# Optimization experiments

Hardware: AMD Instinct MI355X
Metric: run time of the kernel (lower is better)

The kernel has to match this reference:

```python
import jax, jax.numpy as jnp
import numpy as np

WS, SS, IMG, NH = 7, 3, 56, 6  # window, shift, image size, heads
N = WS * WS                    # tokens per window = 49


def _rel_pos_index():
    coords = np.stack(np.meshgrid(np.arange(WS), np.arange(WS), indexing='ij')).reshape(2, -1)
    rel = (coords[:, :, None] - coords[:, None, :]).transpose(1, 2, 0)  # (N,N,2)
    rel[..., 0] += WS - 1
    rel[..., 1] += WS - 1
    rel[..., 0] *= 2 * WS - 1
    return rel.sum(-1)  # (N,N) int


def _attn_mask():
    m = np.zeros((IMG, IMG), np.float32)
    sl = (slice(0, -WS), slice(-WS, -SS), slice(-SS, None))
    cnt = 0
    for hs in sl:
        for ws_ in sl:
            m[hs, ws_] = cnt
            cnt += 1
    mw = m.reshape(IMG // WS, WS, IMG // WS, WS).transpose(0, 2, 1, 3).reshape(-1, N)  # (nW,N)
    diff = mw[:, None, :] - mw[:, :, None]
    return np.where(diff != 0, -100.0, 0.0).astype(np.float32)  # (nW,N,N)


def _ln(x, g, b, eps=1e-5):
    mu = x.mean(-1, keepdims=True)
    var = ((x - mu) ** 2).mean(-1, keepdims=True)
    return (x - mu) * jax.lax.rsqrt(var + eps) * g + b


def reference(x, rpb_table, w_qkv, b_qkv, w_proj, b_proj, g0, be0, g1, be1, w_fc1, b_fc1, w_fc2, b_fc2):
    B, C, _, _ = x.shape
    dh = C // NH
    nWs = IMG // WS
    nW = nWs * nWs

    xs = x.transpose(0, 2, 3, 1)            # NHWC [B,IMG,IMG,C]
    shortcut = xs
    h = _ln(xs, g0, be0)
    h = jnp.roll(h, (-SS, -SS), axis=(1, 2))
    # window partition -> [B*nW, N, C]
    h = h.reshape(B, nWs, WS, nWs, WS, C).transpose(0, 1, 3, 2, 4, 5).reshape(B * nW, N, C)

    qkv = h @ w_qkv.T + b_qkv               # [B_,N,3C]
    qkv = qkv.reshape(B * nW, N, dh, NH, 3)  # matches torch reshape (b_,N,C//h,h,3)
    q = qkv[..., 0].transpose(0, 3, 1, 2) * (dh ** -0.5)  # [B_,H,N,dh]
    k = qkv[..., 1].transpose(0, 3, 1, 2)
    v = qkv[..., 2].transpose(0, 3, 1, 2)

    att = jnp.einsum('bhnd,bhmd->bhnm', q, k)             # [B_,H,N,N]
    bias = rpb_table[jnp.asarray(_rel_pos_index().reshape(-1))].reshape(N, N, NH).transpose(2, 0, 1)
    att = att + bias[None]
    mask = jnp.asarray(_attn_mask())                      # [nW,N,N]
    att = att.reshape(B, nW, NH, N, N) + mask[None, :, None]
    att = jax.nn.softmax(att.reshape(B * nW, NH, N, N), axis=-1)

    o = jnp.einsum('bhnm,bhmd->bnhd', att, v).reshape(B * nW, WS, WS, C)
    o = o @ w_proj.T + b_proj
    # window reverse -> [B,IMG,IMG,C]
    o = o.reshape(B, nWs, nWs, WS, WS, C).transpose(0, 1, 3, 2, 4, 5).reshape(B, IMG, IMG, C)
    o = jnp.roll(o, (SS, SS), axis=(1, 2))

    xs = shortcut + o
    h2 = _ln(xs, g1, be1)
    h2 = jax.nn.gelu(h2 @ w_fc1.T + b_fc1, approximate=False) @ w_fc2.T + b_fc2
    xs = xs + h2
    return xs.transpose(0, 3, 1, 2)  # back to NCHW


def setup_inputs() -> dict:
    key = jax.random.key(0)
    ks = jax.random.split(key, 8)
    C, Hn = 192, 768
    return {
        'x': jax.random.normal(ks[0], (64, C, 56, 56), jnp.float32),
        'rpb_table': jax.random.normal(ks[1], (169, NH), jnp.float32) * 0.02,
        'w_qkv': jax.random.normal(ks[2], (3 * C, C), jnp.float32) * 0.02,
        'b_qkv': jnp.zeros((3 * C,), jnp.float32),
        'w_proj': jax.random.normal(ks[3], (C, C), jnp.float32) * 0.02,
        'b_proj': jnp.zeros((C,), jnp.float32),
        'g0': jnp.ones((C,), jnp.float32),
        'be0': jnp.zeros((C,), jnp.float32),
        'g1': jnp.ones((C,), jnp.float32),
        'be1': jnp.zeros((C,), jnp.float32),
        'w_fc1': jax.random.normal(ks[4], (Hn, C), jnp.float32) * 0.02,
        'b_fc1': jnp.zeros((Hn,), jnp.float32),
        'w_fc2': jax.random.normal(ks[5], (C, Hn), jnp.float32) * 0.02,
        'b_fc2': jnp.zeros((C,), jnp.float32),
    }
```

## Files before the change

kernel.cpp:

```cpp
#include <hip/hip_runtime.h>
#include <hip/hip_bf16.h>

typedef unsigned short ushortT;
typedef __attribute__((ext_vector_type(8))) short short8;
typedef __attribute__((ext_vector_type(4))) float f32x4;
typedef __attribute__((address_space(3))) unsigned int lds_uint;
typedef __attribute__((address_space(1))) const unsigned int glob_uint;

#define MFMA16(a,b,c) __builtin_amdgcn_mfma_f32_16x16x32_bf16(a,b,c,0,0,0)

__device__ __forceinline__ ushortT f2bf(float f){
  union {float f; unsigned u;} v; v.f = f;
  unsigned r = v.u + 0x7FFFu + ((v.u >> 16) & 1u);
  return (ushortT)(r >> 16);
}
__device__ __forceinline__ float bf2f(ushortT u){
  union {unsigned u; float f;} v; v.u = ((unsigned)u) << 16; return v.f;
}
__device__ __forceinline__ float gelu_f(float v){
  float u = 0.7978845608028654f * (v + 0.044715f*v*v*v);
  float e = __expf(2.0f*u);
  return 0.5f * v * (1.0f + (1.0f - 2.0f/(e + 1.0f)));
}

#define SCALE_Q 0.17677669529663687f

__global__ void k_prep(const float* __restrict__ rpb, const float* __restrict__ wqkv,
                       const float* __restrict__ bqkv, const float* __restrict__ wproj,
                       const float* __restrict__ wfc1, const float* __restrict__ wfc2,
                       ushortT* __restrict__ wqkvp, float* __restrict__ bqkvp,
                       ushortT* __restrict__ wprojb, ushortT* __restrict__ wfc1b,
                       ushortT* __restrict__ wfc2b, float* __restrict__ bm)
{
  int i = blockIdx.x * 256 + threadIdx.x;
  if (i < 110592){
    int rp = i / 192, c = i % 192;
    int s = rp / 192, rem = rp % 192, hh = rem / 32, d = rem % 32;
    int rin = d*18 + hh*3 + s;
    float v = wqkv[rin*192 + c];
    if (s == 0) v *= SCALE_Q;
    wqkvp[i] = f2bf(v);
    return;
  }
  i -= 110592;
  if (i < 576){
    int rp = i;
    int s = rp / 192, rem = rp % 192, hh = rem / 32, d = rem % 32;
    int rin = d*18 + hh*3 + s;
    float v = bqkv[rin];
    if (s == 0) v *= SCALE_Q;
    bqkvp[i] = v;
    return;
  }
  i -= 576;
  if (i < 36864){ wprojb[i] = f2bf(wproj[i]); return; }
  i -= 36864;
  if (i < 147456){ wfc1b[i] = f2bf(wfc1[i]); return; }
  i -= 147456;
  if (i < 147456){ wfc2b[i] = f2bf(wfc2[i]); return; }
  i -= 147456;
  if (i < 921984){
    int j = i % 49; int t = i / 49; int ii = t % 49; t /= 49; int hh = t % 6; int w = t / 6;
    int r1 = ii/7, c1 = ii%7, r2 = j/7, c2 = j%7;
    int idx = (r1 - r2 + 6)*13 + (c1 - c2 + 6);
    float bias = rpb[idx*6 + hh];
    int wy = w >> 3, wx = w & 7;
    int hi = wy*7 + r1, wi = wx*7 + c1, hj = wy*7 + r2, wj = wx*7 + c2;
    int regi = 3*((hi<49)?0:((hi<53)?1:2)) + ((wi<49)?0:((wi<53)?1:2));
    int regj = 3*((hj<49)?0:((hj<53)?1:2)) + ((wj<49)?0:((wj<53)?1:2));
    bm[i] = bias + ((regi != regj) ? -100.0f : 0.0f);
  }
}

__global__ void k_tr(const float* __restrict__ x, ushortT* __restrict__ xsb)
{
  __shared__ float tile[192*57];
  int bh = blockIdx.x; int b = bh / 56, h = bh % 56;
  const float* src = x + (size_t)b*602112 + (size_t)h*56;
  for (int e = threadIdx.x; e < 192*56; e += 256){
    int c = e / 56, w = e % 56;
    tile[c*57 + w] = src[(size_t)c*3136 + w];
  }
  __syncthreads();
  ushortT* dst = xsb + (size_t)bh*56*192;
  for (int e = threadIdx.x; e < 56*192; e += 256){
    int w = e / 192, c = e % 192;
    dst[(size_t)w*192 + c] = f2bf(tile[c*57 + w]);
  }
}

__global__ __launch_bounds__(256,2) void k_attn(
  ushortT* __restrict__ xsb, const ushortT* __restrict__ wqkvp, const float* __restrict__ bqkvp,
  const ushortT* __restrict__ wprojb, const float* __restrict__ bproj,
  const float* __restrict__ g0, const float* __restrict__ be0,
  const float* __restrict__ g1, const float* __restrict__ be1,
  const float* __restrict__ bm, ushortT* __restrict__ xs2b)
{
  __shared__ ushortT ln0[49][200];
  __shared__ ushortT ks[49][200];
  __shared__ ushortT vT[6][32][72];
  __shared__ ushortT Pw[4][16][72];

  const int tid = threadIdx.x;
  const int lane = tid & 63, wv = tid >> 6;
  const int l15 = lane & 15, g = lane >> 4;
  const int wid = blockIdx.x;
  const int b = wid >> 6, wloc = wid & 63, wy = wloc >> 3, wx = wloc & 7;
  const int mbase = wv * 16;

  unsigned xr01[13]; ushortT xr2[13];
  #pragma unroll
  for (int it = 0; it < 13; it++){
    int t = wv + it*4;
    if (t < 49){
      int r = t / 7, cc = t % 7;
      int hsrc = (wy*7 + r + 3) % 56;
      int wsrc = (wx*7 + cc + 3) % 56;
      const ushortT* px = xsb + ((size_t)((b*56 + hsrc)*56 + wsrc))*192;
      ushortT r0 = px[lane], r1 = px[lane+64], r2 = px[lane+128];
      xr01[it] = ((unsigned)r1 << 16) | r0; xr2[it] = r2;
      float x0 = bf2f(r0), x1 = bf2f(r1), x2 = bf2f(r2);
      float s = x0 + x1 + x2, sq = x0*x0 + x1*x1 + x2*x2;
      #pragma unroll
      for (int m = 1; m < 64; m <<= 1){ s += __shfl_xor(s, m, 64); sq += __shfl_xor(sq, m, 64); }
      float mu = s * (1.0f/192.0f);
      float var = sq * (1.0f/192.0f) - mu*mu;
      float rs = rsqrtf(var + 1e-5f);
      ln0[t][lane]     = f2bf((x0-mu)*rs*g0[lane]     + be0[lane]);
      ln0[t][lane+64]  = f2bf((x1-mu)*rs*g0[lane+64]  + be0[lane+64]);
      ln0[t][lane+128] = f2bf((x2-mu)*rs*g0[lane+128] + be0[lane+128]);
    }
  }
  __syncthreads();

  {
    short8 a[4][6];
    #pragma unroll
    for (int mt = 0; mt < 4; mt++){
      int ra = mt*16 + l15; if (ra > 48) ra = 48;
      #pragma unroll
      for (int kc = 0; kc < 6; kc++)
        a[mt][kc] = *(const short8*)(&ln0[ra][kc*32 + g*8]);
    }
    __syncthreads();
    for (int ntl = 0; ntl < 9; ntl++){
      int nt = wv*9 + ntl;
      int cp = nt*16 + l15;
      const ushortT* wp = wqkvp + (size_t)cp*192 + g*8;
      short8 bfr[6];
      #pragma unroll
      for (int kc = 0; kc < 6; kc++) bfr[kc] = *(const short8*)(wp + kc*32);
      float bias = bqkvp[cp];
      #pragma unroll
      for (int mt = 0; mt < 4; mt++){
        f32x4 acc = {0.f,0.f,0.f,0.f};
        #pragma unroll
        for (int kc = 0; kc < 6; kc++) acc = MFMA16(a[mt][kc], bfr[kc], acc);
        #pragma unroll
        for (int r = 0; r < 4; r++){
          int tok = mt*16 + g*4 + r;
          float v = acc[r] + bias;
          if (cp < 192)      { if (tok < 49) ln0[tok][cp] = f2bf(v); }
          else if (cp < 384) { if (tok < 49) ks[tok][cp-192] = f2bf(v); }
          else { int c2 = cp - 384; vT[c2>>5][c2&31][tok] = f2bf(v); }
        }
      }
    }
  }
  __syncthreads();

  const int rq = (mbase + l15 > 48) ? 48 : (mbase + l15);
  for (int h = 0; h < 6; h++){
    float bmv[4][4];
    #pragma unroll
    for (int r = 0; r < 4; r++){
      int i = mbase + g*4 + r;
      int ic = (i < 49) ? i : 48;
      const float* bmrow = bm + (((size_t)(wloc*6 + h)*49 + ic)*49);
      #pragma unroll
      for (int jt = 0; jt < 4; jt++){
        int j = jt*16 + l15;
        bmv[r][jt] = (i < 49 && j < 49) ? bmrow[j] : -1e30f;
      }
    }
    short8 aq = *(const short8*)(&ln0[rq][h*32 + g*8]);
    f32x4 sreg[4];
    #pragma unroll
    for (int jt = 0; jt < 4; jt++){
      int rk = jt*16 + l15; if (rk > 48) rk = 48;
      short8 bk = *(const short8*)(&ks[rk][h*32 + g*8]);
      f32x4 z = {0.f,0.f,0.f,0.f};
      sreg[jt] = MFMA16(aq, bk, z);
    }
    #pragma unroll
    for (int r = 0; r < 4; r++){
      float rv[4];
      #pragma unroll
      for (int jt = 0; jt < 4; jt++){
        float bmvv = bmv[r][jt];
        rv[jt] = (bmvv < -1e29f) ? -1e30f : sreg[jt][r] + bmvv;
      }
      float mx = fmaxf(fmaxf(rv[0],rv[1]), fmaxf(rv[2],rv[3]));
      #pragma unroll
      for (int m = 1; m < 16; m <<= 1) mx = fmaxf(mx, __shfl_xor(mx, m, 64));
      float sum = 0.f;
      #pragma unroll
      for (int jt = 0; jt < 4; jt++){ rv[jt] = __expf(rv[jt] - mx); sum += rv[jt]; }
      #pragma unroll
      for (int m = 1; m < 16; m <<= 1) sum += __shfl_xor(sum, m, 64);
      float rden = 1.0f / sum;
      #pragma unroll
      for (int jt = 0; jt < 4; jt++)
        Pw[wv][g*4+r][jt*16 + l15] = f2bf(rv[jt] * rden);
    }
    #pragma unroll
    for (int nt2 = 0; nt2 < 2; nt2++){
      f32x4 oacc = {0.f,0.f,0.f,0.f};
      #pragma unroll
      for (int kk = 0; kk < 2; kk++){
        short8 ap = *(const short8*)(&Pw[wv][l15][kk*32 + g*8]);
        short8 bv = *(const short8*)(&vT[h][nt2*16 + l15][kk*32 + g*8]);
        oacc = MFMA16(ap, bv, oacc);
      }
      #pragma unroll
      for (int r = 0; r < 4; r++){
        int tok = mbase + g*4 + r;
        if (tok < 49) ln0[tok][h*32 + nt2*16 + l15] = f2bf(oacc[r]);
      }
    }
  }
  __syncthreads();

  {
    short8 a2[4][6];
    #pragma unroll
    for (int mt = 0; mt < 4; mt++){
      int ra = mt*16 + l15; if (ra > 48) ra = 48;
      #pragma unroll
      for (int kc = 0; kc < 6; kc++)
        a2[mt][kc] = *(const short8*)(&ln0[ra][kc*32 + g*8]);
    }
    __syncthreads();
    #pragma unroll
    for (int ntl = 0; ntl < 3; ntl++){
      int nt = wv*3 + ntl;
      int cp = nt*16 + l15;
      const ushortT* wp = wprojb + (size_t)cp*192 + g*8;
      short8 bfr[6];
      #pragma unroll
      for (int kc = 0; kc < 6; kc++) bfr[kc] = *(const short8*)(wp + kc*32);
      #pragma unroll
      for (int mt = 0; mt < 4; mt++){
        f32x4 acc = {0.f,0.f,0.f,0.f};
        #pragma unroll
        for (int kc = 0; kc < 6; kc++) acc = MFMA16(a2[mt][kc], bfr[kc], acc);
        #pragma unroll
        for (int r = 0; r < 4; r++){
          int tok = mt*16 + g*4 + r;
          if (tok < 49) ln0[tok][cp] = f2bf(acc[r]);
        }
      }
    }
  }
  __syncthreads();

  #pragma unroll
  for (int it = 0; it < 13; it++){
    int t = wv + it*4;
    if (t < 49){
      int rr = t / 7, cc = t % 7;
      int hdst = (wy*7 + rr + 3) % 56, wdst = (wx*7 + cc + 3) % 56;
      size_t gtok = ((size_t)(b*56 + hdst)*56 + wdst)*192;
      float v0 = bf2f(ln0[t][lane])     + bproj[lane]     + bf2f((ushortT)(xr01[it] & 0xFFFFu));
      float v1 = bf2f(ln0[t][lane+64])  + bproj[lane+64]  + bf2f((ushortT)(xr01[it] >> 16));
      float v2 = bf2f(ln0[t][lane+128]) + bproj[lane+128] + bf2f(xr2[it]);
      float s = v0 + v1 + v2, sq = v0*v0 + v1*v1 + v2*v2;
      #pragma unroll
      for (int m = 1; m < 64; m <<= 1){ s += __shfl_xor(s, m, 64); sq += __shfl_xor(sq, m, 64); }
      float mu = s * (1.0f/192.0f);
      float var = sq * (1.0f/192.0f) - mu*mu;
      float rs = rsqrtf(var + 1e-5f);
      xs2b[gtok + lane]     = f2bf(v0);
      xs2b[gtok + lane+64]  = f2bf(v1);
      xs2b[gtok + lane+128] = f2bf(v2);
      xsb[gtok + lane]     = f2bf((v0-mu)*rs*g1[lane]     + be1[lane]);
      xsb[gtok + lane+64]  = f2bf((v1-mu)*rs*g1[lane+64]  + be1[lane+64]);
      xsb[gtok + lane+128] = f2bf((v2-mu)*rs*g1[lane+128] + be1[lane+128]);
    }
  }
}

__global__ __launch_bounds__(512,4) void k_mlp_fused(
  const ushortT* __restrict__ A,
  const ushortT* __restrict__ w1g,
  const float* __restrict__ b1,
  const ushortT* __restrict__ w2g,
  const float* __restrict__ b2,
  const ushortT* __restrict__ xs2b,
  float* __restrict__ out)
{
  __shared__ ushortT w1s[2][6144];
  __shared__ ushortT w2s[2][6144];
  __shared__ ushortT Hbuf[128][40];

  const int tid = threadIdx.x, lane = tid & 63, wv = tid >> 6;
  const int l15 = lane & 15, g = lane >> 4;
  const size_t Mbase = (size_t)blockIdx.x * 128;
  const int rowb = wv * 16;

  short8 a[6];
  {
    size_t row = Mbase + rowb + l15;
    #pragma unroll
    for (int kc = 0; kc < 6; kc++)
      a[kc] = __builtin_nontemporal_load((const short8*)(A + row*192 + kc*32 + g*8));
  }

  #define STAGE(HB, NB)                                                         \
    _Pragma("unroll")                                                           \
    for (int j = 0; j < 3; j++){                                                \
      int id = wv + j*8;                                                        \
      if (id < 12){                                                             \
        int ci = id;                                                            \
        int q = ci*4 + (lane >> 4);                                             \
        int gq = q & 3, t = q >> 2;                                             \
        int nt = t / 6, kc = t % 6;                                             \
        const ushortT* src = w1g + (size_t)((HB)*32 + nt*16 + (lane & 15))*192  \
                             + kc*32 + gq*8;                                    \
        __builtin_amdgcn_global_load_lds((glob_uint*)src,                       \
            (lds_uint*)(&w1s[NB][ci*512]), 16, 0, 0);                           \
      } else {                                                                  \
        int ci = id - 12;                                                       \
        int q = ci*4 + (lane >> 4);                                             \
        int nt = q >> 2, gq = q & 3;                                            \
        const ushortT* src = w2g + (size_t)(nt*16 + (lane & 15))*768            \
                             + (HB)*32 + gq*8;                                  \
        __builtin_amdgcn_global_load_lds((glob_uint*)src,                       \
            (lds_uint*)(&w2s[NB][ci*512]), 16, 0, 0);                           \
      }                                                                         \
    }

  STAGE(0, 0);
  __syncthreads();

  f32x4 acc2[12];
  #pragma unroll
  for (int nt = 0; nt < 12; nt++) acc2[nt] = (f32x4){0.f,0.f,0.f,0.f};

  for (int hb = 0; hb < 24; hb++){
    const int cb = hb & 1;
    if (hb < 23){ STAGE(hb+1, cb^1); }

    #pragma unroll
    for (int nt = 0; nt < 2; nt++){
      short8 bfr[6];
      #pragma unroll
      for (int kc = 0; kc < 6; kc++){
        int q = (nt*6 + kc)*4 + g;
        bfr[kc] = *(const short8*)(&w1s[cb][(q*16 + l15)*8]);
      }
      float bias = b1[hb*32 + nt*16 + l15];
      f32x4 acc = {0.f,0.f,0.f,0.f};
      #pragma unroll
      for (int kc = 0; kc < 6; kc++) acc = MFMA16(a[kc], bfr[kc], acc);
      #pragma unroll
      for (int r = 0; r < 4; r++)
        Hbuf[rowb + g*4 + r][nt*16 + l15] = f2bf(gelu_f(acc[r] + bias));
    }
    short8 h2f = *(const short8*)(&Hbuf[rowb + l15][g*8]);
    #pragma unroll
    for (int nt = 0; nt < 12; nt++){
      int q2 = nt*4 + g;
      short8 wfr = *(const short8*)(&w2s[cb][(q2*16 + l15)*8]);
      acc2[nt] = MFMA16(h2f, wfr, acc2[nt]);
    }
    __syncthreads();
  }

  #pragma unroll
  for (int nt = 0; nt < 12; nt++){
    int c = nt*16 + l15;
    float bs = b2[c];
    #pragma unroll
    for (int r = 0; r < 4; r++){
      size_t tok = Mbase + rowb + g*4 + r;
      float v = acc2[nt][r] + bs + bf2f(xs2b[tok*192 + c]);
      unsigned t32 = (unsigned)tok;
      unsigned bb = t32 / 3136u, rem = t32 % 3136u;
      out[(size_t)bb*602112 + (size_t)c*3136 + rem] = v;
    }
  }
  #undef STAGE
}

extern "C" void kernel_launch(void* const* d_in, const int* in_sizes, int n_in,
                              void* d_out, int out_size, void* d_ws, size_t ws_size,
                              hipStream_t stream)
{
  const float* x      = (const float*)d_in[0];
  const float* rpb    = (const float*)d_in[1];
  const float* w_qkv  = (const float*)d_in[2];
  const float* b_qkv  = (const float*)d_in[3];
  const float* w_proj = (const float*)d_in[4];
  const float* b_proj = (const float*)d_in[5];
  const float* g0     = (const float*)d_in[6];
  const float* be0    = (const float*)d_in[7];
  const float* g1     = (const float*)d_in[8];
  const float* be1    = (const float*)d_in[9];
  const float* w_fc1  = (const float*)d_in[10];
  const float* b_fc1  = (const float*)d_in[11];
  const float* w_fc2  = (const float*)d_in[12];
  const float* b_fc2  = (const float*)d_in[13];
  float* out = (float*)d_out;
  char* ws = (char*)d_ws;

  ushortT* xsb    = (ushortT*)(ws);
  ushortT* xs2b   = (ushortT*)(ws + 77070336);
  ushortT* wqkvp  = (ushortT*)(ws + 154140672);
  float*   bqkvp  = (float*)(ws + 154361856);
  ushortT* wprojb = (ushortT*)(ws + 154364160);
  ushortT* wfc1b  = (ushortT*)(ws + 154437888);
  ushortT* wfc2b  = (ushortT*)(ws + 154732800);
  float*   bm     = (float*)(ws + 155027712);

  k_prep<<<5332, 256, 0, stream>>>(rpb, w_qkv, b_qkv, w_proj, w_fc1, w_fc2,
                                   wqkvp, bqkvp, wprojb, wfc1b, wfc2b, bm);
  k_tr<<<3584, 256, 0, stream>>>(x, xsb);
  k_attn<<<4096, 256, 0, stream>>>(xsb, wqkvp, bqkvp, wprojb, b_proj,
                                   g0, be0, g1, be1, bm, xs2b);
  k_mlp_fused<<<1568, 512, 0, stream>>>(xsb, wfc1b, b_fc1, wfc2b, b_fc2, xs2b, out);
}
```

Baseline: 708.2 us.

## Split attention into two head halves to shrink LDS and raise occupancy

The k_attn kernel now computes K and V for heads 0-2 first, runs attention on them, then computes K/V for heads 3-5 into the same halved LDS buffers. This roughly halves the K/V shared memory so three blocks can fit per CU, and launch bounds are raised to 3. The residual shortcut is no longer kept in registers; it is re-read from global memory in the epilogue, which frees registers at the cost of extra global reads. The change also adds two more block-wide barriers and keeps the A fragments live across both phases, which may add register pressure.

New measurement: 687.3 us. 1.03x faster.

```diff
diff --git a/kernel.cpp b/kernel.cpp
--- a/kernel.cpp
+++ b/kernel.cpp
@@ -89,7 +89,7 @@
   }
 }
 
-__global__ __launch_bounds__(256,2) void k_attn(
+__global__ __launch_bounds__(256,3) void k_attn(
   ushortT* __restrict__ xsb, const ushortT* __restrict__ wqkvp, const float* __restrict__ bqkvp,
   const ushortT* __restrict__ wprojb, const float* __restrict__ bproj,
   const float* __restrict__ g0, const float* __restrict__ be0,
@@ -97,8 +97,8 @@
   const float* __restrict__ bm, ushortT* __restrict__ xs2b)
 {
   __shared__ ushortT ln0[49][200];
-  __shared__ ushortT ks[49][200];
-  __shared__ ushortT vT[6][32][72];
+  __shared__ ushortT ksh[49][104];
+  __shared__ ushortT vTh[3][32][72];
   __shared__ ushortT Pw[4][16][72];
 
   const int tid = threadIdx.x;
@@ -108,69 +108,63 @@
   const int b = wid >> 6, wloc = wid & 63, wy = wloc >> 3, wx = wloc & 7;
   const int mbase = wv * 16;
 
-  unsigned xr01[13]; ushortT xr2[13];
+  for (int t = wv; t < 49; t += 4){
+    int r = t / 7, cc = t % 7;
+    int hsrc = (wy*7 + r + 3) % 56;
+    int wsrc = (wx*7 + cc + 3) % 56;
+    const ushortT* px = xsb + ((size_t)((b*56 + hsrc)*56 + wsrc))*192;
+    float x0 = bf2f(px[lane]), x1 = bf2f(px[lane+64]), x2 = bf2f(px[lane+128]);
+    float s = x0 + x1 + x2, sq = x0*x0 + x1*x1 + x2*x2;
+    #pragma unroll
+    for (int m = 1; m < 64; m <<= 1){ s += __shfl_xor(s, m, 64); sq += __shfl_xor(sq, m, 64); }
+    float mu = s * (1.0f/192.0f);
+    float var = sq * (1.0f/192.0f) - mu*mu;
+    float rs = rsqrtf(var + 1e-5f);
+    ln0[t][lane]     = f2bf((x0-mu)*rs*g0[lane]     + be0[lane]);
+    ln0[t][lane+64]  = f2bf((x1-mu)*rs*g0[lane+64]  + be0[lane+64]);
+    ln0[t][lane+128] = f2bf((x2-mu)*rs*g0[lane+128] + be0[lane+128]);
+  }
+  __syncthreads();
+
+  short8 a[4][6];
   #pragma unroll
-  for (int it = 0; it < 13; it++){
-    int t = wv + it*4;
-    if (t < 49){
-      int r = t / 7, cc = t % 7;
-      int hsrc = (wy*7 + r + 3) % 56;
-      int wsrc = (wx*7 + cc + 3) % 56;
-      const ushortT* px = xsb + ((size_t)((b*56 + hsrc)*56 + wsrc))*192;
-      ushortT r0 = px[lane], r1 = px[lane+64], r2 = px[lane+128];
-      xr01[it] = ((unsigned)r1 << 16) | r0; xr2[it] = r2;
-      float x0 = bf2f(r0), x1 = bf2f(r1), x2 = bf2f(r2);
-      float s = x0 + x1 + x2, sq = x0*x0 + x1*x1 + x2*x2;
-      #pragma unroll
-      for (int m = 1; m < 64; m <<= 1){ s += __shfl_xor(s, m, 64); sq += __shfl_xor(sq, m, 64); }
-      float mu = s * (1.0f/192.0f);
-      float var = sq * (1.0f/192.0f) - mu*mu;
-      float rs = rsqrtf(var + 1e-5f);
-      ln0[t][lane]     = f2bf((x0-mu)*rs*g0[lane]     + be0[lane]);
-      ln0[t][lane+64]  = f2bf((x1-mu)*rs*g0[lane+64]  + be0[lane+64]);
-      ln0[t][lane+128] = f2bf((x2-mu)*rs*g0[lane+128] + be0[lane+128]);
-    }
-  }
-  __syncthreads();
-
-  {
-    short8 a[4][6];
+  for (int mt = 0; mt < 4; mt++){
+    int ra = mt*16 + l15; if (ra > 48) ra = 48;
+    #pragma unroll
+    for (int kc = 0; kc < 6; kc++)
+      a[mt][kc] = *(const short8*)(&ln0[ra][kc*32 + g*8]);
+  }
+  __syncthreads();
+
+  for (int ntl = 0; ntl < 6; ntl++){
+    int idx = wv*6 + ntl;
+    int nt = (idx < 18) ? idx : idx + 6;
+    int cp = nt*16 + l15;
+    const ushortT* wp = wqkvp + (size_t)cp*192 + g*8;
+    short8 bfr[6];
+    #pragma unroll
+    for (int kc = 0; kc < 6; kc++) bfr[kc] = *(const short8*)(wp + kc*32);
+    float bias = bqkvp[cp];
     #pragma unroll
     for (int mt = 0; mt < 4; mt++){
-      int ra = mt*16 + l15; if (ra > 48) ra = 48;
-      #pragma unroll
-      for (int kc = 0; kc < 6; kc++)
-        a[mt][kc] = *(const short8*)(&ln0[ra][kc*32 + g*8]);
-    }
-    __syncthreads();
-    for (int ntl = 0; ntl < 9; ntl++){
-      int nt = wv*9 + ntl;
-      int cp = nt*16 + l15;
-      const ushortT* wp = wqkvp + (size_t)cp*192 + g*8;
-      short8 bfr[6];
-      #pragma unroll
-      for (int kc = 0; kc < 6; kc++) bfr[kc] = *(const short8*)(wp + kc*32);
-      float bias = bqkvp[cp];
-      #pragma unroll
-      for (int mt = 0; mt < 4; mt++){
-        f32x4 acc = {0.f,0.f,0.f,0.f};
-        #pragma unroll
-        for (int kc = 0; kc < 6; kc++) acc = MFMA16(a[mt][kc], bfr[kc], acc);
-        #pragma unroll
-        for (int r = 0; r < 4; r++){
-          int tok = mt*16 + g*4 + r;
-          float v = acc[r] + bias;
-          if (cp < 192)      { if (tok < 49) ln0[tok][cp] = f2bf(v); }
-          else if (cp < 384) { if (tok < 49) ks[tok][cp-192] = f2bf(v); }
-          else { int c2 = cp - 384; vT[c2>>5][c2&31][tok] = f2bf(v); }
-        }
+      f32x4 acc = {0.f,0.f,0.f,0.f};
+      #pragma unroll
+      for (int kc = 0; kc < 6; kc++) acc = MFMA16(a[mt][kc], bfr[kc], acc);
+      #pragma unroll
+      for (int r = 0; r < 4; r++){
+        int tok = mt*16 + g*4 + r;
+        float v = acc[r] + bias;
+        if (cp < 192)      { if (tok < 49) ln0[tok][cp] = f2bf(v); }
+        else if (cp < 384) { if (tok < 49) ksh[tok][cp-192] = f2bf(v); }
+        else { int c2 = cp - 384; vTh[c2>>5][c2&31][tok] = f2bf(v); }
       }
     }
   }
   __syncthreads();
 
   const int rq = (mbase + l15 > 48) ? 48 : (mbase + l15);
-  for (int h = 0; h < 6; h++){
+  for (int hl = 0; hl < 3; hl++){
+    int h = hl;
     float bmv[4][4];
     #pragma unroll
     for (int r = 0; r < 4; r++){
@@ -188,7 +182,7 @@
     #pragma unroll
     for (int jt = 0; jt < 4; jt++){
       int rk = jt*16 + l15; if (rk > 48) rk = 48;
-      short8 bk = *(const short8*)(&ks[rk][h*32 + g*8]);
+      short8 bk = *(const short8*)(&ksh[rk][hl*32 + g*8]);
       f32x4 z = {0.f,0.f,0.f,0.f};
       sreg[jt] = MFMA16(aq, bk, z);
     }
@@ -219,7 +213,94 @@
       #pragma unroll
       for (int kk = 0; kk < 2; kk++){
         short8 ap = *(const short8*)(&Pw[wv][l15][kk*32 + g*8]);
-        short8 bv = *(const short8*)(&vT[h][nt2*16 + l15][kk*32 + g*8]);
+        short8 bv = *(const short8*)(&vTh[hl][nt2*16 + l15][kk*32 + g*8]);
+        oacc = MFMA16(ap, bv, oacc);
+      }
+      #pragma unroll
+      for (int r = 0; r < 4; r++){
+        int tok = mbase + g*4 + r;
+        if (tok < 49) ln0[tok][h*32 + nt2*16 + l15] = f2bf(oacc[r]);
+      }
+    }
+  }
+  __syncthreads();
+
+  for (int ntl = 0; ntl < 3; ntl++){
+    int idx = wv*3 + ntl;
+    int nt = (idx < 6) ? 18 + idx : 24 + idx;
+    int cp = nt*16 + l15;
+    const ushortT* wp = wqkvp + (size_t)cp*192 + g*8;
+    short8 bfr[6];
+    #pragma unroll
+    for (int kc = 0; kc < 6; kc++) bfr[kc] = *(const short8*)(wp + kc*32);
+    float bias = bqkvp[cp];
+    #pragma unroll
+    for (int mt = 0; mt < 4; mt++){
+      f32x4 acc = {0.f,0.f,0.f,0.f};
+      #pragma unroll
+      for (int kc = 0; kc < 6; kc++) acc = MFMA16(a[mt][kc], bfr[kc], acc);
+      #pragma unroll
+      for (int r = 0; r < 4; r++){
+        int tok = mt*16 + g*4 + r;
+        float v = acc[r] + bias;
+        if (cp < 384) { if (tok < 49) ksh[tok][cp-288] = f2bf(v); }
+        else { int c2 = cp - 480; vTh[c2>>5][c2&31][tok] = f2bf(v); }
+      }
+    }
+  }
+  __syncthreads();
+
+  for (int hl = 0; hl < 3; hl++){
+    int h = 3 + hl;
+    float bmv[4][4];
+    #pragma unroll
+    for (int r = 0; r < 4; r++){
+      int i = mbase + g*4 + r;
+      int ic = (i < 49) ? i : 48;
+      const float* bmrow = bm + (((size_t)(wloc*6 + h)*49 + ic)*49);
+      #pragma unroll
+      for (int jt = 0; jt < 4; jt++){
+        int j = jt*16 + l15;
+        bmv[r][jt] = (i < 49 && j < 49) ? bmrow[j] : -1e30f;
+      }
+    }
+    short8 aq = *(const short8*)(&ln0[rq][h*32 + g*8]);
+    f32x4 sreg[4];
+    #pragma unroll
+    for (int jt = 0; jt < 4; jt++){
+      int rk = jt*16 + l15; if (rk > 48) rk = 48;
+      short8 bk = *(const short8*)(&ksh[rk][hl*32 + g*8]);
+      f32x4 z = {0.f,0.f,0.f,0.f};
+      sreg[jt] = MFMA16(aq, bk, z);
+    }
+    #pragma unroll
+    for (int r = 0; r < 4; r++){
+      float rv[4];
+      #pragma unroll
+      for (int jt = 0; jt < 4; jt++){
+        float bmvv = bmv[r][jt];
+        rv[jt] = (bmvv < -1e29f) ? -1e30f : sreg[jt][r] + bmvv;
+      }
+      float mx = fmaxf(fmaxf(rv[0],rv[1]), fmaxf(rv[2],rv[3]));
+      #pragma unroll
+      for (int m = 1; m < 16; m <<= 1) mx = fmaxf(mx, __shfl_xor(mx, m, 64));
+      float sum = 0.f;
+      #pragma unroll
+      for (int jt = 0; jt < 4; jt++){ rv[jt] = __expf(rv[jt] - mx); sum += rv[jt]; }
+      #pragma unroll
+      for (int m = 1; m < 16; m <<= 1) sum += __shfl_xor(sum, m, 64);
+      float rden = 1.0f / sum;
+      #pragma unroll
+      for (int jt = 0; jt < 4; jt++)
+        Pw[wv][g*4+r][jt*16 + l15] = f2bf(rv[jt] * rden);
+    }
+    #pragma unroll
+    for (int nt2 = 0; nt2 < 2; nt2++){
+      f32x4 oacc = {0.f,0.f,0.f,0.f};
+      #pragma unroll
+      for (int kk = 0; kk < 2; kk++){
+        short8 ap = *(const short8*)(&Pw[wv][l15][kk*32 + g*8]);
+        short8 bv = *(const short8*)(&vTh[hl][nt2*16 + l15][kk*32 + g*8]);
         oacc = MFMA16(ap, bv, oacc);
       }
       #pragma unroll
@@ -264,29 +345,25 @@
   }
   __syncthreads();
 
-  #pragma unroll
-  for (int it = 0; it < 13; it++){
-    int t = wv + it*4;
-    if (t < 49){
-      int rr = t / 7, cc = t % 7;
-      int hdst = (wy*7 + rr + 3) % 56, wdst = (wx*7 + cc + 3) % 56;
-      size_t gtok = ((size_t)(b*56 + hdst)*56 + wdst)*192;
-      float v0 = bf2f(ln0[t][lane])     + bproj[lane]     + bf2f((ushortT)(xr01[it] & 0xFFFFu));
-      float v1 = bf2f(ln0[t][lane+64])  + bproj[lane+64]  + bf2f((ushortT)(xr01[it] >> 16));
-      float v2 = bf2f(ln0[t][lane+128]) + bproj[lane+128] + bf2f(xr2[it]);
-      float s = v0 + v1 + v2, sq = v0*v0 + v1*v1 + v2*v2;
-      #pragma unroll
-      for (int m = 1; m < 64; m <<= 1){ s += __shfl_xor(s, m, 64); sq += __shfl_xor(sq, m, 64); }
-      float mu = s * (1.0f/192.0f);
-      float var = sq * (1.0f/192.0f) - mu*mu;
-      float rs = rsqrtf(var + 1e-5f);
-      xs2b[gtok + lane]     = f2bf(v0);
-      xs2b[gtok + lane+64]  = f2bf(v1);
-      xs2b[gtok + lane+128] = f2bf(v2);
-      xsb[gtok + lane]     = f2bf((v0-mu)*rs*g1[lane]     + be1[lane]);
-      xsb[gtok + lane+64]  = f2bf((v1-mu)*rs*g1[lane+64]  + be1[lane+64]);
-      xsb[gtok + lane+128] = f2bf((v2-mu)*rs*g1[lane+128] + be1[lane+128]);
-    }
+  for (int t = wv; t < 49; t += 4){
+    int rr = t / 7, cc = t % 7;
+    int hdst = (wy*7 + rr + 3) % 56, wdst = (wx*7 + cc + 3) % 56;
+    size_t gtok = ((size_t)(b*56 + hdst)*56 + wdst)*192;
+    float v0 = bf2f(ln0[t][lane])     + bproj[lane]     + bf2f(xsb[gtok + lane]);
+    float v1 = bf2f(ln0[t][lane+64])  + bproj[lane+64]  + bf2f(xsb[gtok + lane+64]);
+    float v2 = bf2f(ln0[t][lane+128]) + bproj[lane+128] + bf2f(xsb[gtok + lane+128]);
+    float s = v0 + v1 + v2, sq = v0*v0 + v1*v1 + v2*v2;
+    #pragma unroll
+    for (int m = 1; m < 64; m <<= 1){ s += __shfl_xor(s, m, 64); sq += __shfl_xor(sq, m, 64); }
+    float mu = s * (1.0f/192.0f);
+    float var = sq * (1.0f/192.0f) - mu*mu;
+    float rs = rsqrtf(var + 1e-5f);
+    xs2b[gtok + lane]     = f2bf(v0);
+    xs2b[gtok + lane+64]  = f2bf(v1);
+    xs2b[gtok + lane+128] = f2bf(v2);
+    xsb[gtok + lane]     = f2bf((v0-mu)*rs*g1[lane]     + be1[lane]);
+    xsb[gtok + lane+64]  = f2bf((v1-mu)*rs*g1[lane+64]  + be1[lane+64]);
+    xsb[gtok + lane+128] = f2bf((v2-mu)*rs*g1[lane+128] + be1[lane+128]);
   }
 }
 
```

## Split attention kernel into head halves to shrink LDS and raise occupancy

Applied to the files above, without the earlier changes.

Restructures the window-attention kernel so K/V are computed and staged for three heads at a time, halving the K and V shared-memory buffers. Q is computed per wave on the fly into the per-wave scratch, and the output projection is accumulated in registers across head halves, so the separate projection pass and its round trip through shared memory go away. Launch bounds move from 2 to 3 blocks per CU. The residual is re-read from global memory instead of being kept in registers. The cost is more global weight loads, since each wave now reloads Q and projection weights per head. A 12-tile register accumulator also adds register pressure.

Result: slower. 975.8 us (+37.8%).

```diff
diff --git a/kernel.cpp b/kernel.cpp
--- a/kernel.cpp
+++ b/kernel.cpp
@@ -89,7 +89,7 @@
   }
 }
 
-__global__ __launch_bounds__(256,2) void k_attn(
+__global__ __launch_bounds__(256,3) void k_attn(
   ushortT* __restrict__ xsb, const ushortT* __restrict__ wqkvp, const float* __restrict__ bqkvp,
   const ushortT* __restrict__ wprojb, const float* __restrict__ bproj,
   const float* __restrict__ g0, const float* __restrict__ be0,
@@ -97,8 +97,8 @@
   const float* __restrict__ bm, ushortT* __restrict__ xs2b)
 {
   __shared__ ushortT ln0[49][200];
-  __shared__ ushortT ks[49][200];
-  __shared__ ushortT vT[6][32][72];
+  __shared__ ushortT ksh[49][104];
+  __shared__ ushortT vTh[3][32][72];
   __shared__ ushortT Pw[4][16][72];
 
   const int tid = threadIdx.x;
@@ -108,184 +108,180 @@
   const int b = wid >> 6, wloc = wid & 63, wy = wloc >> 3, wx = wloc & 7;
   const int mbase = wv * 16;
 
-  unsigned xr01[13]; ushortT xr2[13];
+  for (int t = wv; t < 49; t += 4){
+    int r = t / 7, cc = t % 7;
+    int hsrc = (wy*7 + r + 3) % 56;
+    int wsrc = (wx*7 + cc + 3) % 56;
+    const ushortT* px = xsb + ((size_t)((b*56 + hsrc)*56 + wsrc))*192;
+    float x0 = bf2f(px[lane]), x1 = bf2f(px[lane+64]), x2 = bf2f(px[lane+128]);
+    float s = x0 + x1 + x2, sq = x0*x0 + x1*x1 + x2*x2;
+    #pragma unroll
+    for (int m = 1; m < 64; m <<= 1){ s += __shfl_xor(s, m, 64); sq += __shfl_xor(sq, m, 64); }
+    float mu = s * (1.0f/192.0f);
+    float var = sq * (1.0f/192.0f) - mu*mu;
+    float rs = rsqrtf(var + 1e-5f);
+    ln0[t][lane]     = f2bf((x0-mu)*rs*g0[lane]     + be0[lane]);
+    ln0[t][lane+64]  = f2bf((x1-mu)*rs*g0[lane+64]  + be0[lane+64]);
+    ln0[t][lane+128] = f2bf((x2-mu)*rs*g0[lane+128] + be0[lane+128]);
+  }
+  __syncthreads();
+
+  f32x4 proj_acc[12];
   #pragma unroll
-  for (int it = 0; it < 13; it++){
-    int t = wv + it*4;
-    if (t < 49){
-      int r = t / 7, cc = t % 7;
-      int hsrc = (wy*7 + r + 3) % 56;
-      int wsrc = (wx*7 + cc + 3) % 56;
-      const ushortT* px = xsb + ((size_t)((b*56 + hsrc)*56 + wsrc))*192;
-      ushortT r0 = px[lane], r1 = px[lane+64], r2 = px[lane+128];
-      xr01[it] = ((unsigned)r1 << 16) | r0; xr2[it] = r2;
-      float x0 = bf2f(r0), x1 = bf2f(r1), x2 = bf2f(r2);
-      float s = x0 + x1 + x2, sq = x0*x0 + x1*x1 + x2*x2;
-      #pragma unroll
-      for (int m = 1; m < 64; m <<= 1){ s += __shfl_xor(s, m, 64); sq += __shfl_xor(sq, m, 64); }
-      float mu = s * (1.0f/192.0f);
-      float var = sq * (1.0f/192.0f) - mu*mu;
-      float rs = rsqrtf(var + 1e-5f);
-      ln0[t][lane]     = f2bf((x0-mu)*rs*g0[lane]     + be0[lane]);
-      ln0[t][lane+64]  = f2bf((x1-mu)*rs*g0[lane+64]  + be0[lane+64]);
-      ln0[t][lane+128] = f2bf((x2-mu)*rs*g0[lane+128] + be0[lane+128]);
-    }
-  }
-  __syncthreads();
-
-  {
-    short8 a[4][6];
-    #pragma unroll
-    for (int mt = 0; mt < 4; mt++){
+  for (int nt = 0; nt < 12; nt++) proj_acc[nt] = (f32x4){0.f,0.f,0.f,0.f};
+  const int rq = (mbase + l15 > 48) ? 48 : (mbase + l15);
+
+  for (int hf = 0; hf < 2; hf++){
+    #pragma unroll 1
+    for (int it8 = 0; it8 < 12; it8++){
+      int mt = it8 / 3;
+      int tau = wv*3 + (it8 % 3);
+      int nt = (tau < 6) ? (12 + hf*6 + tau) : (24 + hf*6 + (tau - 6));
+      int cp = nt*16 + l15;
       int ra = mt*16 + l15; if (ra > 48) ra = 48;
-      #pragma unroll
-      for (int kc = 0; kc < 6; kc++)
-        a[mt][kc] = *(const short8*)(&ln0[ra][kc*32 + g*8]);
+      short8 a2[6], bfr[6];
+      #pragma unroll
+      for (int kc = 0; kc < 6; kc++){
+        a2[kc]  = *(const short8*)(&ln0[ra][kc*32 + g*8]);
+        bfr[kc] = *(const short8*)(wqkvp + (size_t)cp*192 + kc*32 + g*8);
+      }
+      float bias = bqkvp[cp];
+      f32x4 acc = {0.f,0.f,0.f,0.f};
+      #pragma unroll
+      for (int kc = 0; kc < 6; kc++) acc = MFMA16(a2[kc], bfr[kc], acc);
+      #pragma unroll
+      for (int r = 0; r < 4; r++){
+        int tok = mt*16 + g*4 + r;
+        float v = acc[r] + bias;
+        if (cp < 384) { if (tok < 49) ksh[tok][cp - 192 - hf*96] = f2bf(v); }
+        else { int c2 = cp - 384 - hf*96; vTh[c2>>5][c2&31][tok] = f2bf(v); }
+      }
     }
     __syncthreads();
-    for (int ntl = 0; ntl < 9; ntl++){
-      int nt = wv*9 + ntl;
+
+    short8 a_own[6];
+    #pragma unroll
+    for (int kc = 0; kc < 6; kc++)
+      a_own[kc] = *(const short8*)(&ln0[rq][kc*32 + g*8]);
+    short8 a_proj[3];
+
+    for (int hl = 0; hl < 3; hl++){
+      int h = hf*3 + hl;
+      float bmv[4][4];
+      #pragma unroll
+      for (int r = 0; r < 4; r++){
+        int i = mbase + g*4 + r;
+        int ic = (i < 49) ? i : 48;
+        const float* bmrow = bm + (((size_t)(wloc*6 + h)*49 + ic)*49);
+        #pragma unroll
+        for (int jt = 0; jt < 4; jt++){
+          int j = jt*16 + l15;
+          bmv[r][jt] = (i < 49 && j < 49) ? bmrow[j] : -1e30f;
+        }
+      }
+      #pragma unroll
+      for (int nq = 0; nq < 2; nq++){
+        int cp = (h*2 + nq)*16 + l15;
+        const ushortT* wp = wqkvp + (size_t)cp*192 + g*8;
+        short8 bq[6];
+        #pragma unroll
+        for (int kc = 0; kc < 6; kc++) bq[kc] = *(const short8*)(wp + kc*32);
+        float qb = bqkvp[cp];
+        f32x4 qacc = {0.f,0.f,0.f,0.f};
+        #pragma unroll
+        for (int kc = 0; kc < 6; kc++) qacc = MFMA16(a_own[kc], bq[kc], qacc);
+        #pragma unroll
+        for (int r = 0; r < 4; r++)
+          Pw[wv][g*4 + r][nq*16 + l15] = f2bf(qacc[r] + qb);
+      }
+      short8 aq = *(const short8*)(&Pw[wv][l15][g*8]);
+      f32x4 sreg[4];
+      #pragma unroll
+      for (int jt = 0; jt < 4; jt++){
+        int rk = jt*16 + l15; if (rk > 48) rk = 48;
+        short8 bk = *(const short8*)(&ksh[rk][hl*32 + g*8]);
+        f32x4 z = {0.f,0.f,0.f,0.f};
+        sreg[jt] = MFMA16(aq, bk, z);
+      }
+      #pragma unroll
+      for (int r = 0; r < 4; r++){
+        float rv[4];
+        #pragma unroll
+        for (int jt = 0; jt < 4; jt++){
+          float bmvv = bmv[r][jt];
+          rv[jt] = (bmvv < -1e29f) ? -1e30f : sreg[jt][r] + bmvv;
+        }
+        float mx = fmaxf(fmaxf(rv[0],rv[1]), fmaxf(rv[2],rv[3]));
+        #pragma unroll
+        for (int m = 1; m < 16; m <<= 1) mx = fmaxf(mx, __shfl_xor(mx, m, 64));
+        float sum = 0.f;
+        #pragma unroll
+        for (int jt = 0; jt < 4; jt++){ rv[jt] = __expf(rv[jt] - mx); sum += rv[jt]; }
+        #pragma unroll
+        for (int m = 1; m < 16; m <<= 1) sum += __shfl_xor(sum, m, 64);
+        float rden = 1.0f / sum;
+        #pragma unroll
+        for (int jt = 0; jt < 4; jt++)
+          Pw[wv][g*4 + r][jt*16 + l15] = f2bf(rv[jt] * rden);
+      }
+      f32x4 oacc[2];
+      #pragma unroll
+      for (int nt2 = 0; nt2 < 2; nt2++){
+        f32x4 z = {0.f,0.f,0.f,0.f};
+        #pragma unroll
+        for (int kk = 0; kk < 2; kk++){
+          short8 ap = *(const short8*)(&Pw[wv][l15][kk*32 + g*8]);
+          short8 bv = *(const short8*)(&vTh[hl][nt2*16 + l15][kk*32 + g*8]);
+          z = MFMA16(ap, bv, z);
+        }
+        oacc[nt2] = z;
+      }
+      #pragma unroll
+      for (int nt2 = 0; nt2 < 2; nt2++)
+        #pragma unroll
+        for (int r = 0; r < 4; r++)
+          Pw[wv][g*4 + r][nt2*16 + l15] = f2bf(oacc[nt2][r]);
+      a_proj[hl] = *(const short8*)(&Pw[wv][l15][g*8]);
+    }
+
+    #pragma unroll
+    for (int nt = 0; nt < 12; nt++){
       int cp = nt*16 + l15;
-      const ushortT* wp = wqkvp + (size_t)cp*192 + g*8;
-      short8 bfr[6];
-      #pragma unroll
-      for (int kc = 0; kc < 6; kc++) bfr[kc] = *(const short8*)(wp + kc*32);
-      float bias = bqkvp[cp];
-      #pragma unroll
-      for (int mt = 0; mt < 4; mt++){
-        f32x4 acc = {0.f,0.f,0.f,0.f};
-        #pragma unroll
-        for (int kc = 0; kc < 6; kc++) acc = MFMA16(a[mt][kc], bfr[kc], acc);
-        #pragma unroll
-        for (int r = 0; r < 4; r++){
-          int tok = mt*16 + g*4 + r;
-          float v = acc[r] + bias;
-          if (cp < 192)      { if (tok < 49) ln0[tok][cp] = f2bf(v); }
-          else if (cp < 384) { if (tok < 49) ks[tok][cp-192] = f2bf(v); }
-          else { int c2 = cp - 384; vT[c2>>5][c2&31][tok] = f2bf(v); }
-        }
-      }
-    }
-  }
-  __syncthreads();
-
-  const int rq = (mbase + l15 > 48) ? 48 : (mbase + l15);
-  for (int h = 0; h < 6; h++){
-    float bmv[4][4];
-    #pragma unroll
-    for (int r = 0; r < 4; r++){
-      int i = mbase + g*4 + r;
-      int ic = (i < 49) ? i : 48;
-      const float* bmrow = bm + (((size_t)(wloc*6 + h)*49 + ic)*49);
-      #pragma unroll
-      for (int jt = 0; jt < 4; jt++){
-        int j = jt*16 + l15;
-        bmv[r][jt] = (i < 49 && j < 49) ? bmrow[j] : -1e30f;
-      }
-    }
-    short8 aq = *(const short8*)(&ln0[rq][h*32 + g*8]);
-    f32x4 sreg[4];
-    #pragma unroll
-    for (int jt = 0; jt < 4; jt++){
-      int rk = jt*16 + l15; if (rk > 48) rk = 48;
-      short8 bk = *(const short8*)(&ks[rk][h*32 + g*8]);
-      f32x4 z = {0.f,0.f,0.f,0.f};
-      sreg[jt] = MFMA16(aq, bk, z);
-    }
-    #pragma unroll
-    for (int r = 0; r < 4; r++){
-      float rv[4];
-      #pragma unroll
-      for (int jt = 0; jt < 4; jt++){
-        float bmvv = bmv[r][jt];
-        rv[jt] = (bmvv < -1e29f) ? -1e30f : sreg[jt][r] + bmvv;
-      }
-      float mx = fmaxf(fmaxf(rv[0],rv[1]), fmaxf(rv[2],rv[3]));
-      #pragma unroll
-      for (int m = 1; m < 16; m <<= 1) mx = fmaxf(mx, __shfl_xor(mx, m, 64));
-      float sum = 0.f;
-      #pragma unroll
-      for (int jt = 0; jt < 4; jt++){ rv[jt] = __expf(rv[jt] - mx); sum += rv[jt]; }
-      #pragma unroll
-      for (int m = 1; m < 16; m <<= 1) sum += __shfl_xor(sum, m, 64);
-      float rden = 1.0f / sum;
-      #pragma unroll
-      for (int jt = 0; jt < 4; jt++)
-        Pw[wv][g*4+r][jt*16 + l15] = f2bf(rv[jt] * rden);
-    }
-    #pragma unroll
-    for (int nt2 = 0; nt2 < 2; nt2++){
-      f32x4 oacc = {0.f,0.f,0.f,0.f};
-      #pragma unroll
-      for (int kk = 0; kk < 2; kk++){
-        short8 ap = *(const short8*)(&Pw[wv][l15][kk*32 + g*8]);
-        short8 bv = *(const short8*)(&vT[h][nt2*16 + l15][kk*32 + g*8]);
-        oacc = MFMA16(ap, bv, oacc);
-      }
-      #pragma unroll
-      for (int r = 0; r < 4; r++){
-        int tok = mbase + g*4 + r;
-        if (tok < 49) ln0[tok][h*32 + nt2*16 + l15] = f2bf(oacc[r]);
-      }
-    }
-  }
-  __syncthreads();
-
-  {
-    short8 a2[4][6];
-    #pragma unroll
-    for (int mt = 0; mt < 4; mt++){
-      int ra = mt*16 + l15; if (ra > 48) ra = 48;
-      #pragma unroll
-      for (int kc = 0; kc < 6; kc++)
-        a2[mt][kc] = *(const short8*)(&ln0[ra][kc*32 + g*8]);
-    }
-    __syncthreads();
-    #pragma unroll
-    for (int ntl = 0; ntl < 3; ntl++){
-      int nt = wv*3 + ntl;
-      int cp = nt*16 + l15;
-      const ushortT* wp = wprojb + (size_t)cp*192 + g*8;
-      short8 bfr[6];
-      #pragma unroll
-      for (int kc = 0; kc < 6; kc++) bfr[kc] = *(const short8*)(wp + kc*32);
-      #pragma unroll
-      for (int mt = 0; mt < 4; mt++){
-        f32x4 acc = {0.f,0.f,0.f,0.f};
-        #pragma unroll
-        for (int kc = 0; kc < 6; kc++) acc = MFMA16(a2[mt][kc], bfr[kc], acc);
-        #pragma unroll
-        for (int r = 0; r < 4; r++){
-          int tok = mt*16 + g*4 + r;
-          if (tok < 49) ln0[tok][cp] = f2bf(acc[r]);
-        }
-      }
-    }
-  }
-  __syncthreads();
+      const ushortT* wp = wprojb + (size_t)cp*192 + (hf*3)*32 + g*8;
+      #pragma unroll
+      for (int hl = 0; hl < 3; hl++){
+        short8 bfr = *(const short8*)(wp + hl*32);
+        proj_acc[nt] = MFMA16(a_proj[hl], bfr, proj_acc[nt]);
+      }
+    }
+    if (hf == 0) __syncthreads();
+  }
 
   #pragma unroll
-  for (int it = 0; it < 13; it++){
-    int t = wv + it*4;
+  for (int r = 0; r < 4; r++){
+    int t = mbase + g*4 + r;
     if (t < 49){
       int rr = t / 7, cc = t % 7;
       int hdst = (wy*7 + rr + 3) % 56, wdst = (wx*7 + cc + 3) % 56;
       size_t gtok = ((size_t)(b*56 + hdst)*56 + wdst)*192;
-      float v0 = bf2f(ln0[t][lane])     + bproj[lane]     + bf2f((ushortT)(xr01[it] & 0xFFFFu));
-      float v1 = bf2f(ln0[t][lane+64])  + bproj[lane+64]  + bf2f((ushortT)(xr01[it] >> 16));
-      float v2 = bf2f(ln0[t][lane+128]) + bproj[lane+128] + bf2f(xr2[it]);
-      float s = v0 + v1 + v2, sq = v0*v0 + v1*v1 + v2*v2;
-      #pragma unroll
-      for (int m = 1; m < 64; m <<= 1){ s += __shfl_xor(s, m, 64); sq += __shfl_xor(sq, m, 64); }
+      float vv[12]; float s = 0.f, sq = 0.f;
+      #pragma unroll
+      for (int nt = 0; nt < 12; nt++){
+        int c = nt*16 + l15;
+        float val = proj_acc[nt][r] + bproj[c] + bf2f(xsb[gtok + c]);
+        vv[nt] = val; s += val; sq += val*val;
+      }
+      #pragma unroll
+      for (int m = 1; m < 16; m <<= 1){ s += __shfl_xor(s, m, 64); sq += __shfl_xor(sq, m, 64); }
       float mu = s * (1.0f/192.0f);
       float var = sq * (1.0f/192.0f) - mu*mu;
       float rs = rsqrtf(var + 1e-5f);
-      xs2b[gtok + lane]     = f2bf(v0);
-      xs2b[gtok + lane+64]  = f2bf(v1);
-      xs2b[gtok + lane+128] = f2bf(v2);
-      xsb[gtok + lane]     = f2bf((v0-mu)*rs*g1[lane]     + be1[lane]);
-      xsb[gtok + lane+64]  = f2bf((v1-mu)*rs*g1[lane+64]  + be1[lane+64]);
-      xsb[gtok + lane+128] = f2bf((v2-mu)*rs*g1[lane+128] + be1[lane+128]);
+      #pragma unroll
+      for (int nt = 0; nt < 12; nt++){
+        int c = nt*16 + l15;
+        xs2b[gtok + c] = f2bf(vv[nt]);
+        xsb[gtok + c]  = f2bf((vv[nt] - mu)*rs*g1[c] + be1[c]);
+      }
     }
   }
 }
```
